# Kernel optimization log

Hardware: AMD Instinct MI355X
Metric: run time of the kernel (lower is better)

Reference implementation:

```python
import jax, jax.numpy as jnp
import numpy as np

D = 2048   # num_vars
H = 4096   # hidden width (2*D, pyro default)
B = 8192   # batch


def _made_masks():
    #   input degrees  : 1..D
    #   hidden degrees : arange(H) % (D-1) + 1  (in 1..D-1)
    #   output degrees : 1..D, strict inequality for the output layer
    inp_deg = np.arange(1, D + 1)
    hid_deg = np.arange(H) % (D - 1) + 1
    out_deg = np.arange(1, D + 1)
    m1 = (hid_deg[:, None] >= inp_deg[None, :]).astype(np.float32)  # [H, D]
    m2 = (hid_deg[:, None] >= hid_deg[None, :]).astype(np.float32)  # [H, H]
    m3 = (out_deg[:, None] > hid_deg[None, :]).astype(np.float32)   # [D, H]
    return jnp.asarray(m1), jnp.asarray(m2), jnp.asarray(m3)

M1, M2, M3 = _made_masks()
PERM = jnp.arange(D)  # permutation=torch.arange(num_vars) -> identity gather


def setup_inputs() -> dict:
    key = jax.random.key(0)
    ks = jax.random.split(key, 7)
    value = jax.random.randint(ks[0], (B, D), 0, 2).astype(jnp.float32)
    s1 = 1.0 / np.sqrt(D)
    s2 = 1.0 / np.sqrt(H)
    W1 = jax.random.uniform(ks[1], (H, D), minval=-s1, maxval=s1, dtype=jnp.float32)
    b1 = jax.random.uniform(ks[2], (H,), minval=-s1, maxval=s1, dtype=jnp.float32)
    W2 = jax.random.uniform(ks[3], (H, H), minval=-s2, maxval=s2, dtype=jnp.float32)
    b2 = jax.random.uniform(ks[4], (H,), minval=-s2, maxval=s2, dtype=jnp.float32)
    W3 = jax.random.uniform(ks[5], (D, H), minval=-s2, maxval=s2, dtype=jnp.float32)
    b3 = jax.random.uniform(ks[6], (D,), minval=-s2, maxval=s2, dtype=jnp.float32)
    return {"value": value, "W1": W1, "b1": b1, "W2": W2, "b2": b2,
            "W3": W3, "b3": b3}


def reference(value, W1, b1, W2, b2, W3, b3):
    h1 = jax.nn.relu(value @ (W1 * M1).T + b1)          # [B, H]
    h2 = jax.nn.relu(h1 @ (W2 * M2).T + b2)             # [B, H]
    logits = h2 @ (W3 * M3).T + b3                      # [B, D]
    logits = logits[:, PERM]                            # identity permutation gather
    # Bernoulli(logits).log_prob(value) = value*logits - softplus(logits)
    log_prob = (value * logits - jax.nn.softplus(logits)).sum(axis=1)  # [B]
    return log_prob
```

## Files before the change

### kernel.cpp

```cpp
#include <hip/hip_runtime.h>
#include <hip/hip_bf16.h>
#include <cstdint>

typedef short short8 __attribute__((ext_vector_type(8)));
typedef float floatx4 __attribute__((ext_vector_type(4)));
typedef float f32x4 __attribute__((ext_vector_type(4)));
typedef unsigned short u16;
typedef unsigned short u16x4 __attribute__((ext_vector_type(4)));

#define BB 8192
#define DD 2048
#define HH 4096

static __device__ __forceinline__ u16 f2bf(float x) {
  __hip_bfloat16 h = __float2bfloat16(x);
  return __builtin_bit_cast(u16, h);
}

static __device__ __forceinline__ float bf2f(u16 x) {
  unsigned int u = ((unsigned int)x) << 16;
  return __builtin_bit_cast(float, u);
}

static __device__ __forceinline__ void glds16(const u16* g, u16* l) {
  __builtin_amdgcn_global_load_lds(
      (const __attribute__((address_space(1))) void*)g,
      (__attribute__((address_space(3))) void*)l, 16, 0, 0);
}

__global__ void cvt_value_kernel(const float* __restrict__ in, u16* __restrict__ out, int n4) {
  int idx = blockIdx.x * blockDim.x + threadIdx.x;
  int stride = gridDim.x * blockDim.x;
  for (int i = idx; i < n4; i += stride) {
    f32x4 v = reinterpret_cast<const f32x4*>(in)[i];
    u16x4 o = { f2bf(v[0]), f2bf(v[1]), f2bf(v[2]), f2bf(v[3]) };
    reinterpret_cast<u16x4*>(out)[i] = o;
  }
}

template<int MODE>
__global__ void mask_cvt_kernel(const float* __restrict__ in, u16* __restrict__ out, int n4) {
  const int shift = (MODE == 0) ? 11 : 12;
  const int cmask = (MODE == 0) ? 2047 : 4095;
  int idx0 = blockIdx.x * blockDim.x + threadIdx.x;
  int stride = gridDim.x * blockDim.x;
  for (int i = idx0; i < n4; i += stride) {
    int e0 = i * 4;
    int row = e0 >> shift;
    int col = e0 & cmask;
    int rdeg = row % 2047;
    f32x4 v = reinterpret_cast<const f32x4*>(in)[i];
    u16x4 o;
#pragma unroll
    for (int e = 0; e < 4; ++e) {
      int c = col + e;
      bool keep;
      if (MODE == 0)      keep = (c <= rdeg);
      else if (MODE == 1) keep = ((c % 2047) <= rdeg);
      else                keep = (row > (c % 2047));
      o[e] = keep ? f2bf(v[e]) : (u16)0;
    }
    reinterpret_cast<u16x4*>(out)[i] = o;
  }
}

template<int MASKM>
__global__ __launch_bounds__(512, 2) void gemm256_kernel(
    const u16* __restrict__ A, const u16* __restrict__ Bw,
    const float* __restrict__ bias, u16* __restrict__ C,
    int M, int N, int K)
{
  __shared__ u16 ls[2][32768];

  const int tid  = threadIdx.x;
  const int wid  = tid >> 6;
  const int lane = tid & 63;
  const int wm = wid >> 2, wn = wid & 3;
  const int l15 = lane & 15, lhi = lane >> 4;
  const int brow = blockIdx.y * 256;
  const int p = blockIdx.x;
  int cols[2];
  cols[0] = (p < 4) ? p : p + 4;
  cols[1] = (p < 4) ? 7 - p : 19 - p;

  const int arow_ = tid >> 3;
  const int agsub = (tid & 7) ^ (arow_ & 7);
  size_t aB[4];
  aB[0] = (size_t)(brow +   0 + arow_) * K + agsub * 8;
  aB[1] = (size_t)(brow + 128 + arow_) * K + agsub * 8;
  aB[2] = (size_t)(brow +  64 + arow_) * K + agsub * 8;
  aB[3] = (size_t)(brow + 192 + arow_) * K + agsub * 8;
  const int aCh[4] = {0, 1024, 512, 1536};

#pragma unroll 1
  for (int t = 0; t < 2; ++t) {
    const int bcol = cols[t] * 256;

    int rmax;
    {
      int sC = bcol, e = bcol + 255;
      if (e <= 2046)       rmax = e;
      else if (sC <= 2046) rmax = 2046;
      else { int em = e - 2047; rmax = (em <= 2046) ? em : 2046; }
    }
    int r1end = ((rmax >> 6) + 1) << 6; if (r1end > K) r1end = K;
    int run2start, r2end;
    if (MASKM == 1) { run2start = r1end; r2end = r1end; }
    else {
      run2start = (1984 > r1end) ? 1984 : r1end;
      r2end = (((2047 + rmax) >> 6) + 1) << 6; if (r2end > K) r2end = K;
      if (r2end < run2start) r2end = run2start;
    }
    const int n1 = r1end >> 6;
    const int nt = n1 + ((r2end - run2start) >> 6);
    const int roff = run2start - r1end;

    size_t bB[2][2];
#pragma unroll
    for (int u = 0; u < 2; ++u)
#pragma unroll
      for (int c = 0; c < 2; ++c)
        bB[u][c] = (size_t)(bcol + u * 128 + arow_ + 64 * c) * K + agsub * 8;

    floatx4 acc[8][4];
#pragma unroll
    for (int i = 0; i < 8; ++i)
#pragma unroll
      for (int j = 0; j < 4; ++j)
        acc[i][j] = (floatx4){0.f, 0.f, 0.f, 0.f};

#define K0F(j) (((j) << 6) + (((j) >= n1) ? roff : 0))
#define ST_A(slot_, idx_, k0v) glds16(A + aB[idx_] + (k0v), (u16*)&ls[slot_][(aCh[idx_] + tid) * 8])
#define ST_B(slot_, u_, k0v) do { \
      glds16(Bw + bB[u_][0] + (k0v), (u16*)&ls[slot_][(2048 + (u_) * 1024 + tid) * 8]); \
      glds16(Bw + bB[u_][1] + (k0v), (u16*)&ls[slot_][(2048 + (u_) * 1024 + tid + 512) * 8]); \
    } while (0)

    ST_A(0, 0, 0); ST_A(0, 1, 0);
    ST_B(0, 0, 0); ST_B(0, 1, 0);
    ST_A(0, 2, 0); ST_A(0, 3, 0);
    if (nt > 1) {
      const int k1p = K0F(1);
      ST_A(1, 0, k1p); ST_A(1, 1, k1p);
      asm volatile("s_waitcnt vmcnt(4)" ::: "memory");
    } else {
      asm volatile("s_waitcnt vmcnt(2)" ::: "memory");
    }
    __builtin_amdgcn_sched_barrier(0);
    __builtin_amdgcn_s_barrier();

#pragma unroll 1
    for (int i = 0; i < nt; ++i) {
      const int s = i & 1, o = s ^ 1;
      const u16* sA = &ls[s][0];
      const u16* sB = &ls[s][16384];
      const bool g1 = (i + 1 < nt), g2 = (i + 2 < nt);
      const int k1 = g1 ? K0F(i + 1) : 0;
      const int k2 = g2 ? K0F(i + 2) : 0;
      short8 af[4], bf0[4], bf1[4];

#define RD_A(q_, ks_) do { \
        _Pragma("unroll") \
        for (int mi = 0; mi < 4; ++mi) { \
          int row = wm * 128 + (q_) * 64 + mi * 16 + l15; \
          int ch = row * 8 + (((ks_) * 4 + lhi) ^ (row & 7)); \
          af[mi] = *(const short8*)&sA[ch * 8]; \
        } } while (0)
#define RD_B(ks_, dst_) do { \
        _Pragma("unroll") \
        for (int ni = 0; ni < 4; ++ni) { \
          int row = wn * 64 + ni * 16 + l15; \
          int ch = row * 8 + (((ks_) * 4 + lhi) ^ (row & 7)); \
          dst_[ni] = *(const short8*)&sB[ch * 8]; \
        } } while (0)
#define MFMA16(q_, bf_) do { \
        _Pragma("unroll") \
        for (int mi = 0; mi < 4; ++mi) \
          _Pragma("unroll") \
          for (int ni = 0; ni < 4; ++ni) \
            acc[(q_) * 4 + mi][ni] = __builtin_amdgcn_mfma_f32_16x16x32_bf16( \
                af[mi], bf_[ni], acc[(q_) * 4 + mi][ni], 0, 0, 0); \
        } while (0)

      RD_A(0, 0);
      RD_B(0, bf0);
      if (g1) ST_B(o, 0, k1);
      __builtin_amdgcn_s_barrier();
      asm volatile("s_waitcnt lgkmcnt(0)" ::: "memory");
      __builtin_amdgcn_sched_barrier(0);
      __builtin_amdgcn_s_setprio(1);
      MFMA16(0, bf0);
      __builtin_amdgcn_s_setprio(0);
      __builtin_amdgcn_s_barrier();

      RD_A(0, 1);
      RD_B(1, bf1);
      if (g1) ST_B(o, 1, k1);
      __builtin_amdgcn_s_barrier();
      asm volatile("s_waitcnt lgkmcnt(0)" ::: "memory");
      __builtin_amdgcn_sched_barrier(0);
      __builtin_amdgcn_s_setprio(1);
      MFMA16(0, bf1);
      __builtin_amdgcn_s_setprio(0);
      if (g1) {
        if (i == 0) asm volatile("s_waitcnt vmcnt(6)" ::: "memory");
        else        asm volatile("s_waitcnt vmcnt(5)" ::: "memory");
      } else {
        asm volatile("s_waitcnt vmcnt(0)" ::: "memory");
      }
      __builtin_amdgcn_sched_barrier(0);
      __builtin_amdgcn_s_barrier();

      RD_A(1, 0);
      if (g1) ST_A(o, 2, k1);
      if (g2) ST_A(s, 0, k2);
      __builtin_amdgcn_s_barrier();
      asm volatile("s_waitcnt lgkmcnt(0)" ::: "memory");
      __builtin_amdgcn_sched_barrier(0);
      __builtin_amdgcn_s_setprio(1);
      MFMA16(1, bf0);
      __builtin_amdgcn_s_setprio(0);
      __builtin_amdgcn_s_barrier();

      RD_A(1, 1);
      if (g1) ST_A(o, 3, k1);
      if (g2) ST_A(s, 1, k2);
      __builtin_amdgcn_s_barrier();
      asm volatile("s_waitcnt lgkmcnt(0)" ::: "memory");
      __builtin_amdgcn_sched_barrier(0);
      __builtin_amdgcn_s_setprio(1);
      MFMA16(1, bf1);
      __builtin_amdgcn_s_setprio(0);
      if (g1) {
        if (g2) asm volatile("s_waitcnt vmcnt(4)" ::: "memory");
        else    asm volatile("s_waitcnt vmcnt(2)" ::: "memory");
        __builtin_amdgcn_sched_barrier(0);
      }
      __builtin_amdgcn_s_barrier();
#undef RD_A
#undef RD_B
#undef MFMA16
    }

#pragma unroll
    for (int mi = 0; mi < 8; ++mi) {
      int row = brow + wm * 128 + (mi >> 2) * 64 + (mi & 3) * 16 + lhi * 4;
#pragma unroll
      for (int ni = 0; ni < 4; ++ni) {
        int col = bcol + wn * 64 + ni * 16 + l15;
        float bv = bias[col];
#pragma unroll
        for (int e = 0; e < 4; ++e) {
          float v = acc[mi][ni][e] + bv;
          v = fmaxf(v, 0.0f);
          C[(size_t)(row + e) * N + col] = f2bf(v);
        }
      }
    }
    __syncthreads();
#undef K0F
#undef ST_A
#undef ST_B
  }
}

__global__ __launch_bounds__(256) void gemm3_kernel(
    const u16* __restrict__ A,
    const u16* __restrict__ Bw,
    const float* __restrict__ bias,
    const u16* __restrict__ vbf,
    float* __restrict__ outp,
    int M, int N, int K)
{
  __shared__ u16 lsA[64 * 64];
  __shared__ u16 lsB[256 * 64];

  const int tid  = threadIdx.x;
  const int wave = tid >> 6;
  const int lane = tid & 63;
  const int wr = wave >> 1;
  const int wc = wave & 1;
  const int l15 = lane & 15;
  const int lhi = lane >> 4;
  const int brow = blockIdx.y * 64;

  const int q = blockIdx.x;
  int sgs[2] = { q, 7 - q };

  size_t aOff[2]; u16* aDst[2];
#pragma unroll
  for (int u = 0; u < 2; ++u) {
    int ch = tid + 256 * u;
    int row = ch >> 3, sub = ch & 7;
    int ssub = sub ^ (row & 7);
    aOff[u] = (size_t)(brow + row) * K + ssub * 8;
    aDst[u] = &lsA[ch * 8];
  }
  int bRow[8], bSsub[8]; u16* bDst[8];
#pragma unroll
  for (int u = 0; u < 8; ++u) {
    int ch = tid + 256 * u;
    int row = ch >> 3, sub = ch & 7;
    bRow[u] = row;
    bSsub[u] = sub ^ (row & 7);
    bDst[u] = &lsB[ch * 8];
  }

#pragma unroll 1
  for (int t = 0; t < 2; ++t) {
    const int sg = sgs[t];
    const int bcol = sg * 256;
    const int rmax = bcol + 254;

    int r1end = ((rmax >> 6) + 1) << 6; if (r1end > K) r1end = K;
    int run2start = (1984 > r1end) ? 1984 : r1end;
    int r2end = (((2047 + rmax) >> 6) + 1) << 6; if (r2end > K) r2end = K;
    if (r2end < run2start) r2end = run2start;
    const int n1 = r1end >> 6;
    const int nt = n1 + ((r2end - run2start) >> 6);
    const int roff = run2start - r1end;

    size_t bOff[8];
#pragma unroll
    for (int u = 0; u < 8; ++u)
      bOff[u] = (size_t)(bcol + bRow[u]) * K + bSsub[u] * 8;

    floatx4 acc[2][8];
#pragma unroll
    for (int i = 0; i < 2; ++i)
#pragma unroll
      for (int j = 0; j < 8; ++j)
        acc[i][j] = (floatx4){0.f, 0.f, 0.f, 0.f};

#pragma unroll 1
    for (int i = 0; i < nt; ++i) {
      const int k0 = (i << 6) + ((i >= n1) ? roff : 0);
#pragma unroll
      for (int u = 0; u < 2; ++u) glds16(A + aOff[u] + k0, aDst[u]);
#pragma unroll
      for (int u = 0; u < 8; ++u) glds16(Bw + bOff[u] + k0, bDst[u]);
      __syncthreads();

#pragma unroll
      for (int ks = 0; ks < 2; ++ks) {
        short8 af[2], bfv[8];
#pragma unroll
        for (int mi = 0; mi < 2; ++mi) {
          int row = wr * 32 + mi * 16 + l15;
          af[mi] = *(const short8*)&lsA[row * 64 + (((ks * 4 + lhi) ^ (row & 7)) * 8)];
        }
#pragma unroll
        for (int ni = 0; ni < 8; ++ni) {
          int row = wc * 128 + ni * 16 + l15;
          bfv[ni] = *(const short8*)&lsB[row * 64 + (((ks * 4 + lhi) ^ (row & 7)) * 8)];
        }
#pragma unroll
        for (int mi = 0; mi < 2; ++mi)
#pragma unroll
          for (int ni = 0; ni < 8; ++ni)
            acc[mi][ni] = __builtin_amdgcn_mfma_f32_16x16x32_bf16(af[mi], bfv[ni], acc[mi][ni], 0, 0, 0);
      }
      __syncthreads();
    }

#pragma unroll
    for (int mi = 0; mi < 2; ++mi) {
#pragma unroll
      for (int e = 0; e < 4; ++e) {
        int row = brow + wr * 32 + mi * 16 + lhi * 4 + e;
        float partial = 0.0f;
#pragma unroll
        for (int ni = 0; ni < 8; ++ni) {
          int col = bcol + wc * 128 + ni * 16 + l15;
          float l = acc[mi][ni][e] + bias[col];
          float v = bf2f(vbf[(size_t)row * DD + col]);
          float sp = fmaxf(l, 0.0f) + __logf(1.0f + __expf(-fabsf(l)));
          partial += v * l - sp;
        }
#pragma unroll
        for (int off = 1; off < 16; off <<= 1)
          partial += __shfl_xor(partial, off, 64);
        if (l15 == 0) atomicAdd(&outp[row], partial);
      }
    }
  }
}

extern "C" void kernel_launch(void* const* d_in, const int* in_sizes, int n_in,
                              void* d_out, int out_size, void* d_ws, size_t ws_size,
                              hipStream_t stream) {
  const float* value = (const float*)d_in[0];
  const float* W1 = (const float*)d_in[1];
  const float* b1 = (const float*)d_in[2];
  const float* W2 = (const float*)d_in[3];
  const float* b2 = (const float*)d_in[4];
  const float* W3 = (const float*)d_in[5];
  const float* b3 = (const float*)d_in[6];
  float* out = (float*)d_out;

  char* ws = (char*)d_ws;
  u16* vbf = (u16*)(ws);
  u16* w1m = (u16*)(ws + 33554432ULL);
  u16* w2m = (u16*)(ws + 50331648ULL);
  u16* w3m = (u16*)(ws + 83886080ULL);
  u16* h1  = (u16*)(ws + 100663296ULL);
  u16* h2  = (u16*)(ws + 167772160ULL);

  hipMemsetAsync(d_out, 0, (size_t)out_size * sizeof(float), stream);

  cvt_value_kernel<<<2048, 256, 0, stream>>>(value, vbf, (BB * DD) / 4);
  mask_cvt_kernel<0><<<2048, 256, 0, stream>>>(W1, w1m, (HH * DD) / 4);
  mask_cvt_kernel<1><<<2048, 256, 0, stream>>>(W2, w2m, (HH * HH) / 4);
  mask_cvt_kernel<2><<<2048, 256, 0, stream>>>(W3, w3m, (DD * HH) / 4);

  dim3 g12(8, BB / 256);
  gemm256_kernel<1><<<g12, 512, 0, stream>>>(vbf, w1m, b1, h1, BB, HH, DD);
  gemm256_kernel<2><<<g12, 512, 0, stream>>>(h1, w2m, b2, h2, BB, HH, HH);
  dim3 g3(4, BB / 64);
  gemm3_kernel<<<g3, 256, 0, stream>>>(h2, w3m, b3, vbf, out, BB, DD, HH);
}
```

Baseline: 402.6 us.

## Tile masked weight conversion, add wrap-around K tile, pipeline layer-3 GEMM

The weight mask-and-convert kernels are rewritten as 64x64 tiled kernels. Tiles that are entirely masked out skip reading the fp32 source and just write zeros. The layer-2 GEMM now also processes the last K tile (K-64), which holds the hidden units whose degree wraps past 2047, so the mask skipping no longer drops them. The layer-3 GEMM is rebuilt with 512 threads, 128x256 tiles, double-buffered LDS, prefetch of the next tile and setprio around the MFMAs, to overlap global loads with compute. The cost is one extra K iteration per block, plus more LDS and registers per block in the layer-3 kernel.

```diff
diff --git a/kernel.cpp b/kernel.cpp
--- a/kernel.cpp
+++ b/kernel.cpp
@@ -39,28 +39,56 @@
 }
 
 template<int MODE>
-__global__ void mask_cvt_kernel(const float* __restrict__ in, u16* __restrict__ out, int n4) {
-  const int shift = (MODE == 0) ? 11 : 12;
-  const int cmask = (MODE == 0) ? 2047 : 4095;
-  int idx0 = blockIdx.x * blockDim.x + threadIdx.x;
-  int stride = gridDim.x * blockDim.x;
-  for (int i = idx0; i < n4; i += stride) {
-    int e0 = i * 4;
-    int row = e0 >> shift;
-    int col = e0 & cmask;
-    int rdeg = row % 2047;
-    f32x4 v = reinterpret_cast<const f32x4*>(in)[i];
+__global__ __launch_bounds__(256) void mask_cvt_tile(const float* __restrict__ in,
+                                                     u16* __restrict__ out, int W) {
+  const int r0 = blockIdx.y * 64;
+  const int c0 = blockIdx.x * 64;
+  const int re = r0 + 63, ce = c0 + 63;
+
+  bool zero;
+  if (MODE == 0) {
+    int rmaxd = (r0 >= 2047) ? ((re <= 4093) ? (re - 2047) : 2046)
+                             : ((re <= 2046) ? re : 2046);
+    zero = (c0 > rmaxd);
+  } else if (MODE == 1) {
+    int rmaxd = (r0 >= 2047) ? ((re <= 4093) ? (re - 2047) : 2046)
+                             : ((re <= 2046) ? re : 2046);
+    int cmind = (c0 >= 2047) ? ((ce >= 4094) ? 0 : (c0 - 2047))
+                             : ((ce >= 2047) ? 0 : c0);
+    zero = (cmind > rmaxd);
+  } else {
+    int cmind = (c0 >= 2047) ? ((ce >= 4094) ? 0 : (c0 - 2047))
+                             : ((ce >= 2047) ? 0 : c0);
+    zero = (re <= cmind);
+  }
+
+  const int tr = threadIdx.x >> 4;
+  const int tc = (threadIdx.x & 15) * 4;
+
+  if (zero) {
+    u16x4 z = {0, 0, 0, 0};
+#pragma unroll
+    for (int rr = 0; rr < 64; rr += 16)
+      *(u16x4*)&out[(size_t)(r0 + tr + rr) * W + c0 + tc] = z;
+    return;
+  }
+
+#pragma unroll
+  for (int rr = 0; rr < 64; rr += 16) {
+    int r = r0 + tr + rr;
+    int rdeg = r % 2047;
+    f32x4 v = *(const f32x4*)&in[(size_t)r * W + c0 + tc];
     u16x4 o;
 #pragma unroll
     for (int e = 0; e < 4; ++e) {
-      int c = col + e;
+      int c = c0 + tc + e;
       bool keep;
       if (MODE == 0)      keep = (c <= rdeg);
       else if (MODE == 1) keep = ((c % 2047) <= rdeg);
-      else                keep = (row > (c % 2047));
+      else                keep = (r > (c % 2047));
       o[e] = keep ? f2bf(v[e]) : (u16)0;
     }
-    reinterpret_cast<u16x4*>(out)[i] = o;
+    *(u16x4*)&out[(size_t)r * W + c0 + tc] = o;
   }
 }
 
@@ -114,6 +142,7 @@
     const int n1 = r1end >> 6;
     const int nt = n1 + ((r2end - run2start) >> 6);
     const int roff = run2start - r1end;
+    const int nte = nt + ((MASKM != 1 && r2end < K) ? 1 : 0);
 
     size_t bB[2][2];
 #pragma unroll
@@ -129,17 +158,17 @@
       for (int j = 0; j < 4; ++j)
         acc[i][j] = (floatx4){0.f, 0.f, 0.f, 0.f};
 
-#define K0F(j) (((j) << 6) + (((j) >= n1) ? roff : 0))
+#define K0F(j) (((j) >= nt) ? (K - 64) : (((j) << 6) + (((j) >= n1) ? roff : 0)))
 #define ST_A(slot_, idx_, k0v) glds16(A + aB[idx_] + (k0v), (u16*)&ls[slot_][(aCh[idx_] + tid) * 8])
 #define ST_B(slot_, u_, k0v) do { \
       glds16(Bw + bB[u_][0] + (k0v), (u16*)&ls[slot_][(2048 + (u_) * 1024 + tid) * 8]); \
       glds16(Bw + bB[u_][1] + (k0v), (u16*)&ls[slot_][(2048 + (u_) * 1024 + tid + 512) * 8]); \
     } while (0)
 
-    ST_A(0, 0, 0); ST_A(0, 1, 0);
-    ST_B(0, 0, 0); ST_B(0, 1, 0);
-    ST_A(0, 2, 0); ST_A(0, 3, 0);
-    if (nt > 1) {
+    ST_A(0, 0, K0F(0)); ST_A(0, 1, K0F(0));
+    ST_B(0, 0, K0F(0)); ST_B(0, 1, K0F(0));
+    ST_A(0, 2, K0F(0)); ST_A(0, 3, K0F(0));
+    if (nte > 1) {
       const int k1p = K0F(1);
       ST_A(1, 0, k1p); ST_A(1, 1, k1p);
       asm volatile("s_waitcnt vmcnt(4)" ::: "memory");
@@ -150,11 +179,11 @@
     __builtin_amdgcn_s_barrier();
 
 #pragma unroll 1
-    for (int i = 0; i < nt; ++i) {
+    for (int i = 0; i < nte; ++i) {
       const int s = i & 1, o = s ^ 1;
       const u16* sA = &ls[s][0];
       const u16* sB = &ls[s][16384];
-      const bool g1 = (i + 1 < nt), g2 = (i + 2 < nt);
+      const bool g1 = (i + 1 < nte), g2 = (i + 2 < nte);
       const int k1 = g1 ? K0F(i + 1) : 0;
       const int k2 = g2 ? K0F(i + 2) : 0;
       short8 af[4], bf0[4], bf1[4];
@@ -264,7 +293,7 @@
   }
 }
 
-__global__ __launch_bounds__(256) void gemm3_kernel(
+__global__ __launch_bounds__(512, 1) void gemm3p_kernel(
     const u16* __restrict__ A,
     const u16* __restrict__ Bw,
     const float* __restrict__ bias,
@@ -272,44 +301,35 @@
     float* __restrict__ outp,
     int M, int N, int K)
 {
-  __shared__ u16 lsA[64 * 64];
-  __shared__ u16 lsB[256 * 64];
+  __shared__ u16 ls[2][24576];
 
   const int tid  = threadIdx.x;
-  const int wave = tid >> 6;
+  const int wid  = tid >> 6;
   const int lane = tid & 63;
-  const int wr = wave >> 1;
-  const int wc = wave & 1;
-  const int l15 = lane & 15;
-  const int lhi = lane >> 4;
-  const int brow = blockIdx.y * 64;
-
+  const int wm = wid >> 2, wn = wid & 3;
+  const int l15 = lane & 15, lhi = lane >> 4;
+  const int brow = blockIdx.y * 128;
   const int q = blockIdx.x;
   int sgs[2] = { q, 7 - q };
 
-  size_t aOff[2]; u16* aDst[2];
+  size_t aOff[2];
 #pragma unroll
   for (int u = 0; u < 2; ++u) {
-    int ch = tid + 256 * u;
+    int ch = tid + 512 * u;
     int row = ch >> 3, sub = ch & 7;
-    int ssub = sub ^ (row & 7);
-    aOff[u] = (size_t)(brow + row) * K + ssub * 8;
-    aDst[u] = &lsA[ch * 8];
-  }
-  int bRow[8], bSsub[8]; u16* bDst[8];
-#pragma unroll
-  for (int u = 0; u < 8; ++u) {
-    int ch = tid + 256 * u;
-    int row = ch >> 3, sub = ch & 7;
-    bRow[u] = row;
-    bSsub[u] = sub ^ (row & 7);
-    bDst[u] = &lsB[ch * 8];
+    aOff[u] = (size_t)(brow + row) * K + (sub ^ (row & 7)) * 8;
+  }
+  int bRow[4], bSsub[4];
+#pragma unroll
+  for (int u = 0; u < 4; ++u) {
+    int ch = tid + 512 * u;
+    bRow[u] = ch >> 3;
+    bSsub[u] = (ch & 7) ^ (bRow[u] & 7);
   }
 
 #pragma unroll 1
   for (int t = 0; t < 2; ++t) {
-    const int sg = sgs[t];
-    const int bcol = sg * 256;
+    const int bcol = sgs[t] * 256;
     const int rmax = bcol + 254;
 
     int r1end = ((rmax >> 6) + 1) << 6; if (r1end > K) r1end = K;
@@ -319,61 +339,106 @@
     const int n1 = r1end >> 6;
     const int nt = n1 + ((r2end - run2start) >> 6);
     const int roff = run2start - r1end;
-
-    size_t bOff[8];
-#pragma unroll
-    for (int u = 0; u < 8; ++u)
+    const int nte = nt + ((r2end < K) ? 1 : 0);
+
+    size_t bOff[4];
+#pragma unroll
+    for (int u = 0; u < 4; ++u)
       bOff[u] = (size_t)(bcol + bRow[u]) * K + bSsub[u] * 8;
 
-    floatx4 acc[2][8];
-#pragma unroll
-    for (int i = 0; i < 2; ++i)
-#pragma unroll
-      for (int j = 0; j < 8; ++j)
+    floatx4 acc[4][4];
+#pragma unroll
+    for (int i = 0; i < 4; ++i)
+#pragma unroll
+      for (int j = 0; j < 4; ++j)
         acc[i][j] = (floatx4){0.f, 0.f, 0.f, 0.f};
 
+#define K0G(j) (((j) >= nt) ? (K - 64) : (((j) << 6) + (((j) >= n1) ? roff : 0)))
+#define ST3(slot_, k0v) do { \
+      glds16(A  + aOff[0] + (k0v), (u16*)&ls[slot_][tid * 8]); \
+      glds16(A  + aOff[1] + (k0v), (u16*)&ls[slot_][(512 + tid) * 8]); \
+      glds16(Bw + bOff[0] + (k0v), (u16*)&ls[slot_][(1024 + tid) * 8]); \
+      glds16(Bw + bOff[1] + (k0v), (u16*)&ls[slot_][(1536 + tid) * 8]); \
+      glds16(Bw + bOff[2] + (k0v), (u16*)&ls[slot_][(2048 + tid) * 8]); \
+      glds16(Bw + bOff[3] + (k0v), (u16*)&ls[slot_][(2560 + tid) * 8]); \
+    } while (0)
+
+    ST3(0, K0G(0));
+    asm volatile("s_waitcnt vmcnt(0)" ::: "memory");
+    __builtin_amdgcn_sched_barrier(0);
+    __builtin_amdgcn_s_barrier();
+
 #pragma unroll 1
-    for (int i = 0; i < nt; ++i) {
-      const int k0 = (i << 6) + ((i >= n1) ? roff : 0);
-#pragma unroll
-      for (int u = 0; u < 2; ++u) glds16(A + aOff[u] + k0, aDst[u]);
-#pragma unroll
-      for (int u = 0; u < 8; ++u) glds16(Bw + bOff[u] + k0, bDst[u]);
-      __syncthreads();
-
-#pragma unroll
-      for (int ks = 0; ks < 2; ++ks) {
-        short8 af[2], bfv[8];
-#pragma unroll
-        for (int mi = 0; mi < 2; ++mi) {
-          int row = wr * 32 + mi * 16 + l15;
-          af[mi] = *(const short8*)&lsA[row * 64 + (((ks * 4 + lhi) ^ (row & 7)) * 8)];
-        }
-#pragma unroll
-        for (int ni = 0; ni < 8; ++ni) {
-          int row = wc * 128 + ni * 16 + l15;
-          bfv[ni] = *(const short8*)&lsB[row * 64 + (((ks * 4 + lhi) ^ (row & 7)) * 8)];
-        }
-#pragma unroll
-        for (int mi = 0; mi < 2; ++mi)
-#pragma unroll
-          for (int ni = 0; ni < 8; ++ni)
-            acc[mi][ni] = __builtin_amdgcn_mfma_f32_16x16x32_bf16(af[mi], bfv[ni], acc[mi][ni], 0, 0, 0);
-      }
-      __syncthreads();
-    }
-
-#pragma unroll
-    for (int mi = 0; mi < 2; ++mi) {
+    for (int i = 0; i < nte; ++i) {
+      const int s = i & 1, o = s ^ 1;
+      const u16* sA = &ls[s][0];
+      const u16* sB = &ls[s][8192];
+      const bool g1 = (i + 1 < nte);
+      short8 af[4], bfv[4];
+
+#pragma unroll
+      for (int mi = 0; mi < 4; ++mi) {
+        int row = wm * 64 + mi * 16 + l15;
+        af[mi] = *(const short8*)&sA[(row * 8 + (lhi ^ (row & 7))) * 8];
+      }
+#pragma unroll
+      for (int ni = 0; ni < 4; ++ni) {
+        int row = wn * 64 + ni * 16 + l15;
+        bfv[ni] = *(const short8*)&sB[(row * 8 + (lhi ^ (row & 7))) * 8];
+      }
+      if (g1) ST3(o, K0G(i + 1));
+      __builtin_amdgcn_s_barrier();
+      asm volatile("s_waitcnt lgkmcnt(0)" ::: "memory");
+      __builtin_amdgcn_sched_barrier(0);
+      __builtin_amdgcn_s_setprio(1);
+#pragma unroll
+      for (int mi = 0; mi < 4; ++mi)
+#pragma unroll
+        for (int ni = 0; ni < 4; ++ni)
+          acc[mi][ni] = __builtin_amdgcn_mfma_f32_16x16x32_bf16(af[mi], bfv[ni], acc[mi][ni], 0, 0, 0);
+      __builtin_amdgcn_s_setprio(0);
+      __builtin_amdgcn_s_barrier();
+
+#pragma unroll
+      for (int mi = 0; mi < 4; ++mi) {
+        int row = wm * 64 + mi * 16 + l15;
+        af[mi] = *(const short8*)&sA[(row * 8 + ((4 + lhi) ^ (row & 7))) * 8];
+      }
+#pragma unroll
+      for (int ni = 0; ni < 4; ++ni) {
+        int row = wn * 64 + ni * 16 + l15;
+        bfv[ni] = *(const short8*)&sB[(row * 8 + ((4 + lhi) ^ (row & 7))) * 8];
+      }
+      __builtin_amdgcn_s_barrier();
+      asm volatile("s_waitcnt lgkmcnt(0)" ::: "memory");
+      __builtin_amdgcn_sched_barrier(0);
+      __builtin_amdgcn_s_setprio(1);
+#pragma unroll
+      for (int mi = 0; mi < 4; ++mi)
+#pragma unroll
+        for (int ni = 0; ni < 4; ++ni)
+          acc[mi][ni] = __builtin_amdgcn_mfma_f32_16x16x32_bf16(af[mi], bfv[ni], acc[mi][ni], 0, 0, 0);
+      __builtin_amdgcn_s_setprio(0);
+      if (g1) {
+        asm volatile("s_waitcnt vmcnt(0)" ::: "memory");
+        __builtin_amdgcn_sched_barrier(0);
+      }
+      __builtin_amdgcn_s_barrier();
+    }
+#undef K0G
+#undef ST3
+
+#pragma unroll
+    for (int mi = 0; mi < 4; ++mi) {
 #pragma unroll
       for (int e = 0; e < 4; ++e) {
-        int row = brow + wr * 32 + mi * 16 + lhi * 4 + e;
+        int row = brow + wm * 64 + mi * 16 + lhi * 4 + e;
         float partial = 0.0f;
 #pragma unroll
-        for (int ni = 0; ni < 8; ++ni) {
-          int col = bcol + wc * 128 + ni * 16 + l15;
+        for (int ni = 0; ni < 4; ++ni) {
+          int col = bcol + wn * 64 + ni * 16 + l15;
           float l = acc[mi][ni][e] + bias[col];
-          float v = bf2f(vbf[(size_t)row * DD + col]);
+          float v = bf2f(vbf[(size_t)row * N + col]);
           float sp = fmaxf(l, 0.0f) + __logf(1.0f + __expf(-fabsf(l)));
           partial += v * l - sp;
         }
@@ -409,13 +474,13 @@
   hipMemsetAsync(d_out, 0, (size_t)out_size * sizeof(float), stream);
 
   cvt_value_kernel<<<2048, 256, 0, stream>>>(value, vbf, (BB * DD) / 4);
-  mask_cvt_kernel<0><<<2048, 256, 0, stream>>>(W1, w1m, (HH * DD) / 4);
-  mask_cvt_kernel<1><<<2048, 256, 0, stream>>>(W2, w2m, (HH * HH) / 4);
-  mask_cvt_kernel<2><<<2048, 256, 0, stream>>>(W3, w3m, (DD * HH) / 4);
+  mask_cvt_tile<0><<<dim3(DD / 64, HH / 64), 256, 0, stream>>>(W1, w1m, DD);
+  mask_cvt_tile<1><<<dim3(HH / 64, HH / 64), 256, 0, stream>>>(W2, w2m, HH);
+  mask_cvt_tile<2><<<dim3(HH / 64, DD / 64), 256, 0, stream>>>(W3, w3m, HH);
 
   dim3 g12(8, BB / 256);
   gemm256_kernel<1><<<g12, 512, 0, stream>>>(vbf, w1m, b1, h1, BB, HH, DD);
   gemm256_kernel<2><<<g12, 512, 0, stream>>>(h1, w2m, b2, h2, BB, HH, HH);
-  dim3 g3(4, BB / 64);
-  gemm3_kernel<<<g3, 256, 0, stream>>>(h2, w3m, b3, vbf, out, BB, DD, HH);
-}
+  dim3 g3(4, BB / 128);
+  gemm3p_kernel<<<g3, 512, 0, stream>>>(h2, w3m, b3, vbf, out, BB, DD, HH);
+}
```

After: 395.6 us. About the same (-1.7%).
